# Optimization experiments

Hardware: AMD Instinct MI355X
Metric: run time of the kernel (lower is better)

## Reference

```python
import jax, jax.numpy as jnp
import numpy as np

EPS = 1e-12  # undefined global `eps` in the original source; standard tiny epsilon


def setup_inputs() -> dict:
    key = jax.random.key(0)
    k1, k2 = jax.random.split(key)
    B, C = 32768, 1000
    output = jax.random.normal(k1, (B, C), dtype=jnp.float32)
    multilabels = (jax.random.uniform(k2, (B, C)) < 0.05).astype(jnp.float32)
    multilabels = multilabels.at[:, 0].set(1.0)
    return {"output": output, "multilabels": multilabels}


def reference(output, multilabels):
    # Equivalent closed form of: for every nonempty subset g of true labels,
    #   loss(g) = -[ pseudo_y*log(o+eps) + (1-pseudo_y)*log(1-o+eps) ].sum()
    #           = base - sum_{j in g} gain_j,
    # with base = -sum_j log(1-o_j+eps) and gain_j = log(o_j+eps)-log(1-o_j+eps).
    # min over nonempty subsets = base - max nonempty-subset gain
    #   = base - (sum of positive gains over true labels, or the max single
    #      gain among true labels if all gains are negative).
    o = jax.nn.sigmoid(output)                      # [B, C]
    log_p = jnp.log(o + EPS)
    log_np = jnp.log(1.0 - o + EPS)
    base = -jnp.sum(log_np, axis=1)                 # [B]
    gain = log_p - log_np                           # [B, C]
    is_true = multilabels == 1.0                    # [B, C] bool (constant)
    pos = is_true & (gain > 0)
    pos_gain = jnp.sum(jnp.where(pos, gain, 0.0), axis=1)          # [B]
    any_pos = jnp.any(pos, axis=1)                                  # [B]
    best_single = jnp.max(jnp.where(is_true, gain, -jnp.inf), axis=1)  # [B]
    max_gain = jnp.where(any_pos, pos_gain, best_single)
    per_sample = base - max_gain                    # [B]
    return jnp.mean(per_sample)
```

## Files before the change

### kernel.cpp

```cpp
#include <hip/hip_runtime.h>
#include <math.h>


constexpr int B = 32768;
constexpr int C = 1000;
constexpr int C4 = C / 4;
constexpr int THREADS = 256;
constexpr int WAVES_PER_BLOCK = THREADS / 64;
constexpr int ROWS_PER_WAVE = 8;
constexpr int NBLOCKS = B / (WAVES_PER_BLOCK * ROWS_PER_WAVE);

typedef float f32x4 __attribute__((ext_vector_type(4)));

__device__ __forceinline__ void elem_update(float x, float m,
                                            float& base, float& pos, float& best) {
    float e  = __expf(-fabsf(x));
    float xp = fmaxf(x, 0.0f);
    base += xp + __logf(1.0f + e);
    pos  += m * xp;
    if (m != 0.0f) best = fmaxf(best, x);
}

__device__ __forceinline__ void load_row(const float* __restrict__ Xrow,
                                         const float* __restrict__ Mrow,
                                         int lane,
                                         f32x4 (&xb)[4], f32x4 (&mb)[4]) {
    const f32x4* x4 = reinterpret_cast<const f32x4*>(Xrow);
    const f32x4* m4 = reinterpret_cast<const f32x4*>(Mrow);
    #pragma unroll
    for (int j = 0; j < 4; ++j) {
        const int idx = j * 64 + lane;
        if (idx < C4) {
            xb[j] = __builtin_nontemporal_load(x4 + idx);
            mb[j] = __builtin_nontemporal_load(m4 + idx);
        }
    }
}

__device__ __forceinline__ float row_result(int lane,
                                            const f32x4 (&xb)[4],
                                            const f32x4 (&mb)[4]) {
    float base = 0.f, pos = 0.f, best = -INFINITY;
    #pragma unroll
    for (int j = 0; j < 4; ++j) {
        const int idx = j * 64 + lane;
        if (idx < C4) {
            elem_update(xb[j].x, mb[j].x, base, pos, best);
            elem_update(xb[j].y, mb[j].y, base, pos, best);
            elem_update(xb[j].z, mb[j].z, base, pos, best);
            elem_update(xb[j].w, mb[j].w, base, pos, best);
        }
    }
    #pragma unroll
    for (int off = 32; off > 0; off >>= 1) {
        base += __shfl_down(base, off, 64);
        pos  += __shfl_down(pos,  off, 64);
        best  = fmaxf(best, __shfl_down(best, off, 64));
    }
    return base - ((pos > 0.f) ? pos : best);
}

__global__ __launch_bounds__(THREADS)
void row_loss_kernel(const float* __restrict__ X,
                     const float* __restrict__ M,
                     float* __restrict__ partial) {
    const int wid  = blockIdx.x * WAVES_PER_BLOCK + (threadIdx.x >> 6);
    const int lane = threadIdx.x & 63;
    const int row0 = wid * ROWS_PER_WAVE;

    f32x4 xa[4], ma[4], xc[4], mc[4];

    load_row(X + (size_t)row0 * C, M + (size_t)row0 * C, lane, xa, ma);

    #pragma unroll
    for (int k = 0; k < ROWS_PER_WAVE; ++k) {
        const int r = row0 + k;
        if (k + 1 < ROWS_PER_WAVE) {
            const float* Xn = X + (size_t)(r + 1) * C;
            const float* Mn = M + (size_t)(r + 1) * C;
            if (k & 1) load_row(Xn, Mn, lane, xa, ma);
            else       load_row(Xn, Mn, lane, xc, mc);
        }
        const float res = (k & 1) ? row_result(lane, xc, mc)
                                  : row_result(lane, xa, ma);
        if (lane == 0) partial[r] = res;
    }
}

__global__ __launch_bounds__(256)
void finalize1_kernel(const float* __restrict__ partial, float* __restrict__ mid) {
    const int b = blockIdx.x;
    const int t = threadIdx.x;
    float v = partial[b * 512 + t] + partial[b * 512 + t + 256];

    #pragma unroll
    for (int off = 32; off > 0; off >>= 1)
        v += __shfl_down(v, off, 64);

    __shared__ float s[4];
    const int w    = t >> 6;
    const int lane = t & 63;
    if (lane == 0) s[w] = v;
    __syncthreads();
    if (t == 0) mid[b] = (s[0] + s[1]) + (s[2] + s[3]);
}

__global__ __launch_bounds__(64)
void finalize2_kernel(const float* __restrict__ mid, float* __restrict__ out) {
    double v = (double)mid[threadIdx.x];
    #pragma unroll
    for (int off = 32; off > 0; off >>= 1)
        v += __shfl_down(v, off, 64);
    if (threadIdx.x == 0) out[0] = (float)(v / (double)B);
}

extern "C" void kernel_launch(void* const* d_in, const int* in_sizes, int n_in,
                              void* d_out, int out_size, void* d_ws, size_t ws_size,
                              hipStream_t stream) {
    const float* X  = (const float*)d_in[0];
    const float* M  = (const float*)d_in[1];
    float* out      = (float*)d_out;
    float* partial  = (float*)d_ws;
    float* mid      = partial + B;

    row_loss_kernel<<<NBLOCKS, THREADS, 0, stream>>>(X, M, partial);
    finalize1_kernel<<<64, 256, 0, stream>>>(partial, mid);
    finalize2_kernel<<<1, 64, 0, stream>>>(mid, out);
}
```

Before: 251.2 us.

## Split waves between register loads and direct global-to-LDS DMA loads

Two of the four waves in each block now stream their rows through global_load_lds into double-buffered LDS, using explicit vmcnt waits. The other two waves keep the register-prefetch path. The mix is meant to put more loads in flight with less register pressure, which would raise effective HBM bandwidth on this memory-bound reduction. The cost is 32KB of LDS per block, which may limit occupancy, plus hand-written waitcnt sequencing that depends on compiler scheduling.

```diff
diff --git a/kernel.cpp b/kernel.cpp
--- a/kernel.cpp
+++ b/kernel.cpp
@@ -1,16 +1,21 @@
 #include <hip/hip_runtime.h>
 #include <math.h>
+#include <stdint.h>
 
 
 constexpr int B = 32768;
 constexpr int C = 1000;
 constexpr int C4 = C / 4;
 constexpr int THREADS = 256;
-constexpr int WAVES_PER_BLOCK = THREADS / 64;
-constexpr int ROWS_PER_WAVE = 8;
-constexpr int NBLOCKS = B / (WAVES_PER_BLOCK * ROWS_PER_WAVE);
+constexpr int WAVES_PER_BLOCK = 4;
+constexpr int NBLOCKS = 2048;
+constexpr int TOTAL_WAVES = NBLOCKS * WAVES_PER_BLOCK;
+constexpr int ROWS_PER_WAVE = B / TOTAL_WAVES;
+constexpr int DMA_WAVES = 2;
 
 typedef float f32x4 __attribute__((ext_vector_type(4)));
+typedef __attribute__((address_space(3))) void lds_void_t;
+typedef const __attribute__((address_space(1))) void gbl_void_t;
 
 __device__ __forceinline__ void elem_update(float x, float m,
                                             float& base, float& pos, float& best) {
@@ -21,10 +26,21 @@
     if (m != 0.0f) best = fmaxf(best, x);
 }
 
-__device__ __forceinline__ void load_row(const float* __restrict__ Xrow,
-                                         const float* __restrict__ Mrow,
-                                         int lane,
-                                         f32x4 (&xb)[4], f32x4 (&mb)[4]) {
+__device__ __forceinline__ float finish_row(float base, float pos, float best) {
+    #pragma unroll
+    for (int off = 32; off > 0; off >>= 1) {
+        base += __shfl_down(base, off, 64);
+        pos  += __shfl_down(pos,  off, 64);
+        best  = fmaxf(best, __shfl_down(best, off, 64));
+    }
+    return base - ((pos > 0.f) ? pos : best);
+}
+
+
+__device__ __forceinline__ void load_row_nt(const float* __restrict__ Xrow,
+                                            const float* __restrict__ Mrow,
+                                            int lane,
+                                            f32x4 (&xb)[4], f32x4 (&mb)[4]) {
     const f32x4* x4 = reinterpret_cast<const f32x4*>(Xrow);
     const f32x4* m4 = reinterpret_cast<const f32x4*>(Mrow);
     #pragma unroll
@@ -37,9 +53,9 @@
     }
 }
 
-__device__ __forceinline__ float row_result(int lane,
-                                            const f32x4 (&xb)[4],
-                                            const f32x4 (&mb)[4]) {
+__device__ __forceinline__ float row_result_reg(int lane,
+                                                const f32x4 (&xb)[4],
+                                                const f32x4 (&mb)[4]) {
     float base = 0.f, pos = 0.f, best = -INFINITY;
     #pragma unroll
     for (int j = 0; j < 4; ++j) {
@@ -51,39 +67,96 @@
             elem_update(xb[j].w, mb[j].w, base, pos, best);
         }
     }
-    #pragma unroll
-    for (int off = 32; off > 0; off >>= 1) {
-        base += __shfl_down(base, off, 64);
-        pos  += __shfl_down(pos,  off, 64);
-        best  = fmaxf(best, __shfl_down(best, off, 64));
-    }
-    return base - ((pos > 0.f) ? pos : best);
+    return finish_row(base, pos, best);
+}
+
+
+__device__ __forceinline__ void gld_lds16(const void* gsrc, void* ldst) {
+    __builtin_amdgcn_global_load_lds((gbl_void_t*)gsrc, (lds_void_t*)ldst,
+                                     16, 0, 0);
+}
+
+__device__ __forceinline__ void issue_row_dma(const float* __restrict__ Xrow,
+                                              const float* __restrict__ Mrow,
+                                              int lane,
+                                              float* ldsx, float* ldsm) {
+    const f32x4* x4 = reinterpret_cast<const f32x4*>(Xrow);
+    const f32x4* m4 = reinterpret_cast<const f32x4*>(Mrow);
+    #pragma unroll
+    for (int j = 0; j < 4; ++j) {
+        const int idx = min(j * 64 + lane, C4 - 1);
+        gld_lds16((const void*)(x4 + idx), (void*)(ldsx + j * 256));
+        gld_lds16((const void*)(m4 + idx), (void*)(ldsm + j * 256));
+    }
+}
+
+__device__ __forceinline__ float row_result_lds(int lane,
+                                                const float* ldsx,
+                                                const float* ldsm) {
+    float base = 0.f, pos = 0.f, best = -INFINITY;
+    #pragma unroll
+    for (int j = 0; j < 4; ++j) {
+        const int idx = j * 64 + lane;
+        if (idx < C4) {
+            f32x4 x = *reinterpret_cast<const f32x4*>(ldsx + j * 256 + lane * 4);
+            f32x4 m = *reinterpret_cast<const f32x4*>(ldsm + j * 256 + lane * 4);
+            elem_update(x.x, m.x, base, pos, best);
+            elem_update(x.y, m.y, base, pos, best);
+            elem_update(x.z, m.z, base, pos, best);
+            elem_update(x.w, m.w, base, pos, best);
+        }
+    }
+    return finish_row(base, pos, best);
 }
 
 __global__ __launch_bounds__(THREADS)
 void row_loss_kernel(const float* __restrict__ X,
                      const float* __restrict__ M,
                      float* __restrict__ partial) {
-    const int wid  = blockIdx.x * WAVES_PER_BLOCK + (threadIdx.x >> 6);
+    __shared__ __align__(16) float ldsX[DMA_WAVES][2][1024];
+    __shared__ __align__(16) float ldsM[DMA_WAVES][2][1024];
+
+    const int w    = threadIdx.x >> 6;
     const int lane = threadIdx.x & 63;
+    const int wid  = blockIdx.x * WAVES_PER_BLOCK + w;
     const int row0 = wid * ROWS_PER_WAVE;
 
-    f32x4 xa[4], ma[4], xc[4], mc[4];
-
-    load_row(X + (size_t)row0 * C, M + (size_t)row0 * C, lane, xa, ma);
-
-    #pragma unroll
-    for (int k = 0; k < ROWS_PER_WAVE; ++k) {
-        const int r = row0 + k;
-        if (k + 1 < ROWS_PER_WAVE) {
-            const float* Xn = X + (size_t)(r + 1) * C;
-            const float* Mn = M + (size_t)(r + 1) * C;
-            if (k & 1) load_row(Xn, Mn, lane, xa, ma);
-            else       load_row(Xn, Mn, lane, xc, mc);
-        }
-        const float res = (k & 1) ? row_result(lane, xc, mc)
-                                  : row_result(lane, xa, ma);
-        if (lane == 0) partial[r] = res;
+    if (w < 2) {
+        f32x4 xa[4], ma[4], xc[4], mc[4];
+        load_row_nt(X + (size_t)row0 * C, M + (size_t)row0 * C, lane, xa, ma);
+        #pragma unroll
+        for (int k = 0; k < ROWS_PER_WAVE; ++k) {
+            const int r = row0 + k;
+            if (k + 1 < ROWS_PER_WAVE) {
+                const float* Xn = X + (size_t)(r + 1) * C;
+                const float* Mn = M + (size_t)(r + 1) * C;
+                if (k & 1) load_row_nt(Xn, Mn, lane, xa, ma);
+                else       load_row_nt(Xn, Mn, lane, xc, mc);
+            }
+            const float res = (k & 1) ? row_result_reg(lane, xc, mc)
+                                      : row_result_reg(lane, xa, ma);
+            if (lane == 0) partial[r] = res;
+        }
+    } else {
+        const int dw = w - 2;
+        issue_row_dma(X + (size_t)row0 * C, M + (size_t)row0 * C, lane,
+                      &ldsX[dw][0][0], &ldsM[dw][0][0]);
+        #pragma unroll
+        for (int k = 0; k < ROWS_PER_WAVE; ++k) {
+            const int r   = row0 + k;
+            const int cur = k & 1;
+            if (k + 1 < ROWS_PER_WAVE) {
+                issue_row_dma(X + (size_t)(r + 1) * C, M + (size_t)(r + 1) * C,
+                              lane, &ldsX[dw][cur ^ 1][0], &ldsM[dw][cur ^ 1][0]);
+                asm volatile("s_waitcnt vmcnt(8)" ::: "memory");
+            } else {
+                asm volatile("s_waitcnt vmcnt(0)" ::: "memory");
+            }
+            __builtin_amdgcn_sched_barrier(0);
+            const float res = row_result_lds(lane, &ldsX[dw][cur][0],
+                                             &ldsM[dw][cur][0]);
+            if (lane == 0) partial[r] = res;
+        }
     }
 }
 
```

Measured after the change: 269.9 us. 1.07x slower.
